# Performance work log

Hardware: AMD Instinct MI355X
Metric: run time of the kernel (lower is better)

## Reference

```python
import jax, jax.numpy as jnp
import numpy as np
from jax import lax

B, N_BASES, C_IN, C_OUT, K, HW = 32, 5, 128, 128, 3, 56

def setup_inputs() -> dict:
    key = jax.random.key(0)
    k1, k2, k3 = jax.random.split(key, 3)
    x = jax.random.normal(k1, (B, C_IN, HW, HW), dtype=jnp.float32)
    weights = jax.random.normal(k2, (N_BASES, C_OUT, C_IN, K, K), dtype=jnp.float32) * 0.05
    scales = jax.random.uniform(k3, (N_BASES,), dtype=jnp.float32)
    return {"x": x, "weights": weights, "scales": scales}

def _binarize(w):
    # per-base: sign(w) * mean(|w|) over the whole weight tensor of that base
    m = jnp.mean(jnp.abs(w), axis=(1, 2, 3, 4), keepdims=True)  # [N,1,1,1,1]
    return jnp.sign(w) * m

def reference(x, weights, scales):
    # torch pads with constant value 1 (not zero) once, then all bases share it
    xp = jnp.pad(x, ((0, 0), (0, 0), (1, 1), (1, 1)), constant_values=1.0)
    wq = _binarize(weights)                              # [N,O,I,K,K]
    wf = wq.reshape(N_BASES * C_OUT, C_IN, K, K)          # fuse bases into one conv
    out = lax.conv_general_dilated(
        xp, wf, window_strides=(1, 1), padding='VALID',
        dimension_numbers=('NCHW', 'OIHW', 'NCHW'))      # [B, N*O, H, W]
    out = out.reshape(B, N_BASES, C_OUT, HW, HW)
    return jnp.einsum('bnohw,n->bohw', out, scales)
```

## Files before the change

### kernel.cpp

```cpp
#include <hip/hip_runtime.h>
#include <stdint.h>

#define N_BASES 5
#define WELEM (128 * 128 * 3 * 3)

typedef __attribute__((ext_vector_type(4))) float f32x4;
typedef __attribute__((ext_vector_type(8))) short bf16x8;

__device__ __forceinline__ unsigned short f2bf(float v) {
  union { float f; uint32_t u; } un;
  un.f = v;
  uint32_t r = un.u + 0x7FFFu + ((un.u >> 16) & 1u);
  return (unsigned short)(r >> 16);
}

__device__ __forceinline__ void glds16(const void* g, void* l) {
  __builtin_amdgcn_global_load_lds(
      (const __attribute__((address_space(1))) void*)g,
      (__attribute__((address_space(3))) void*)l, 16, 0, 0);
}

__global__ __launch_bounds__(256) void prep_fused(
    const float* __restrict__ x, const float* __restrict__ w,
    unsigned short* __restrict__ xp, float* __restrict__ csum_part) {
  int bi = blockIdx.x;
  if (bi >= 1856) {
    int id = bi - 1856;
    int n = id >> 6;
    int chunk = id & 63;
    const f32x4* wb = (const f32x4*)(w + (size_t)n * WELEM + chunk * 2304);
    float s = 0.f;
    for (int i = threadIdx.x; i < 576; i += 256) {
      f32x4 v = wb[i];
      s += fabsf(v.x) + fabsf(v.y) + fabsf(v.z) + fabsf(v.w);
    }
    #pragma unroll
    for (int off = 32; off > 0; off >>= 1) s += __shfl_down(s, off);
    __shared__ float red[4];
    if ((threadIdx.x & 63) == 0) red[threadIdx.x >> 6] = s;
    __syncthreads();
    if (threadIdx.x == 0) csum_part[id] = red[0] + red[1] + red[2] + red[3];
    return;
  }
  int b = bi / 58;
  int hp = bi - b * 58;
  unsigned short* dst = xp + ((size_t)b * 58 + hp) * 58 * 128;
  int gh = hp - 1;
  if ((unsigned)gh >= 56u) {
    uint4 ones = make_uint4(0x3F803F80u, 0x3F803F80u, 0x3F803F80u, 0x3F803F80u);
    for (int i = threadIdx.x; i < 928; i += 256) ((uint4*)dst)[i] = ones;
    return;
  }
  __shared__ unsigned short tile[128][61];
  const float* src = x + ((size_t)b * 128 * 56 + gh) * 56;
  for (int i = threadIdx.x; i < 128 * 14; i += 256) {
    int c = i / 14;
    int k = i - c * 14;
    f32x4 v = *(const f32x4*)(src + (size_t)c * 3136 + k * 4);
    tile[c][1 + 4 * k + 0] = f2bf(v.x);
    tile[c][1 + 4 * k + 1] = f2bf(v.y);
    tile[c][1 + 4 * k + 2] = f2bf(v.z);
    tile[c][1 + 4 * k + 3] = f2bf(v.w);
  }
  if (threadIdx.x < 128) {
    tile[threadIdx.x][0] = 0x3F80;
    tile[threadIdx.x][57] = 0x3F80;
  }
  __syncthreads();
  for (int i = threadIdx.x; i < 928; i += 256) {
    int wp = i >> 4;
    int c8 = i & 15;
    union { uint4 q; unsigned short h[8]; } u;
    #pragma unroll
    for (int j = 0; j < 8; ++j) u.h[j] = tile[c8 * 8 + j][wp];
    *(uint4*)(dst + (size_t)wp * 128 + c8 * 8) = u.q;
  }
}

__global__ __launch_bounds__(256) void binweight_kernel(
    const float* __restrict__ w, const float* __restrict__ csum_part,
    const float* __restrict__ scales, unsigned short* __restrict__ wq) {
  __shared__ float parts[320];
  __shared__ float coef[N_BASES];
  for (int i = threadIdx.x; i < 320; i += 256) parts[i] = csum_part[i];
  __syncthreads();
  if (threadIdx.x < N_BASES) {
    float s = 0.f;
    #pragma unroll 8
    for (int k = 0; k < 64; ++k) s += parts[threadIdx.x * 64 + k];
    coef[threadIdx.x] = scales[threadIdx.x] * s * (1.0f / (float)WELEM);
  }
  __syncthreads();
  int f = blockIdx.x * 256 + threadIdx.x;
  float s = 0.f;
  #pragma unroll
  for (int n = 0; n < N_BASES; ++n) {
    float cn = coef[n];
    float v = w[n * WELEM + f];
    s += (v > 0.f) ? cn : ((v < 0.f) ? -cn : 0.f);
  }
  int o = f / 1152;
  int rem = f - o * 1152;
  int i = rem / 9;
  int t = rem - i * 9;
  int half = i >> 6;
  int c8 = (i >> 3) & 7;
  int e = i & 7;
  wq[(size_t)(t * 2 + half) * 8192 + o * 64 + ((c8 ^ (o & 7)) << 3) + e] = f2bf(s);
}

__global__ __launch_bounds__(256, 2) void conv_kernel(
    const unsigned short* __restrict__ xp, const unsigned short* __restrict__ wq,
    float* __restrict__ out) {
  __shared__ unsigned short patch[27648];
  __shared__ unsigned short btile[8192];

  const int tid = threadIdx.x;
  const int blk = blockIdx.x;
  const int pair = blk & 15;
  const int tileIdx = blk >> 4;
  const int hi = tileIdx >> 2;
  const int wi = tileIdx & 3;
  const int h0 = hi * 4;
  const int w0 = (wi == 3) ? 40 : wi * 16;

  const size_t rowstride = 58 * 128;
  for (int i = tid; i < 3456; i += 256) {
    int img = i / 1728;
    int r = i - img * 1728;
    int sp = r >> 4;
    int c16 = r & 15;
    int ph = sp / 18;
    int pw = sp - ph * 18;
    int b = pair + img * 16;
    const unsigned short* gp = xp + ((size_t)b * 58 + (h0 + ph)) * rowstride +
                               (size_t)(w0 + pw) * 128 + c16 * 8;
    uint4 v = *(const uint4*)gp;
    *(uint4*)&patch[img * 13824 + sp * 128 + ((c16 ^ (sp & 7)) << 3)] = v;
  }

  const int lane = tid & 63;
  const int wave = tid >> 6;
  const int img = wave >> 1;
  const int nh = wave & 1;
  const int l15 = lane & 15;
  const int quad = lane >> 4;

  f32x4 acc[4][4];
  #pragma unroll
  for (int mf = 0; mf < 4; ++mf)
    #pragma unroll
    for (int nf = 0; nf < 4; ++nf) acc[mf][nf] = (f32x4)0.f;

  const unsigned short* pb = &patch[img * 13824];

  #pragma unroll
  for (int t = 0; t < 9; ++t) {
    const int kh = t / 3;
    const int kw = t - kh * 3;
    int sp_mf[4];
    #pragma unroll
    for (int mf = 0; mf < 4; ++mf) sp_mf[mf] = (mf + kh) * 18 + (l15 + kw);
    #pragma unroll
    for (int half = 0; half < 2; ++half) {
      __syncthreads();
      {
        const unsigned short* g =
            wq + (size_t)(t * 2 + half) * 8192 + wave * 2048 + lane * 8;
        unsigned short* l = &btile[wave * 2048];
        #pragma unroll
        for (int j = 0; j < 4; ++j) glds16(g + j * 512, l + j * 512);
      }
      __syncthreads();
      #pragma unroll
      for (int kk = 0; kk < 2; ++kk) {
        const int kb = half * 2 + kk;
        bf16x8 af[4], bf[4];
        #pragma unroll
        for (int mf = 0; mf < 4; ++mf) {
          int sp = sp_mf[mf];
          af[mf] = *(const bf16x8*)&pb[sp * 128 + (((kb * 4 + quad) ^ (sp & 7)) << 3)];
        }
        #pragma unroll
        for (int nf = 0; nf < 4; ++nf) {
          int o = nh * 64 + nf * 16 + l15;
          bf[nf] = *(const bf16x8*)&btile[o * 64 + (((kk * 4 + quad) ^ (o & 7)) << 3)];
        }
        #pragma unroll
        for (int mf = 0; mf < 4; ++mf)
          #pragma unroll
          for (int nf = 0; nf < 4; ++nf)
            acc[mf][nf] = __builtin_amdgcn_mfma_f32_16x16x32_bf16(
                af[mf], bf[nf], acc[mf][nf], 0, 0, 0);
      }
    }
  }

  const int b = pair + img * 16;
  #pragma unroll
  for (int mf = 0; mf < 4; ++mf) {
    int h = h0 + mf;
    #pragma unroll
    for (int nf = 0; nf < 4; ++nf) {
      int o = nh * 64 + nf * 16 + l15;
      float* p = out + (((size_t)b * 128 + o) * 56 + h) * 56 + w0 + quad * 4;
      *(f32x4*)p = acc[mf][nf];
    }
  }
}

extern "C" void kernel_launch(void* const* d_in, const int* in_sizes, int n_in,
                              void* d_out, int out_size, void* d_ws, size_t ws_size,
                              hipStream_t stream) {
  const float* x = (const float*)d_in[0];
  const float* w = (const float*)d_in[1];
  const float* scales = (const float*)d_in[2];
  float* out = (float*)d_out;

  float* csum_part = (float*)d_ws;
  unsigned short* wq = (unsigned short*)((char*)d_ws + 4096);
  unsigned short* xpad = (unsigned short*)((char*)d_ws + 512 * 1024);

  prep_fused<<<1856 + 320, 256, 0, stream>>>(x, w, xpad, csum_part);
  binweight_kernel<<<576, 256, 0, stream>>>(w, csum_part, scales, wq);
  conv_kernel<<<56 * 16, 256, 0, stream>>>(xpad, wq, out);
}
```

Measured before the change: 152.4 us.

## Double-buffer conv weight tiles and retile blocks to one image by eight rows

Each conv block now covers one image and an 8-row output tile instead of two images at 4 rows each. This shrinks the input patch, since the halo rows are now shared across more output rows. Weight slices are double-buffered in LDS: the next slice is fetched with global_load_lds while the current one is consumed by MFMAs, and a single waitcnt plus barrier per step replaces the two __syncthreads. LDS use per block rises somewhat, and correctness now depends on the manual vmcnt wait and barrier placement.

Result: faster. 148.3 us (-2.7%).

```diff
diff --git a/kernel.cpp b/kernel.cpp
--- a/kernel.cpp
+++ b/kernel.cpp
@@ -112,36 +112,42 @@
 __global__ __launch_bounds__(256, 2) void conv_kernel(
     const unsigned short* __restrict__ xp, const unsigned short* __restrict__ wq,
     float* __restrict__ out) {
-  __shared__ unsigned short patch[27648];
-  __shared__ unsigned short btile[8192];
+  __shared__ unsigned short patch[23040];
+  __shared__ unsigned short btile[2][8192];
 
   const int tid = threadIdx.x;
   const int blk = blockIdx.x;
-  const int pair = blk & 15;
-  const int tileIdx = blk >> 4;
-  const int hi = tileIdx >> 2;
-  const int wi = tileIdx & 3;
-  const int h0 = hi * 4;
+  const int b = blk & 31;
+  const int tile = blk >> 5;
+  const int hi = tile >> 2;
+  const int wi = tile & 3;
+  const int h0 = hi * 8;
   const int w0 = (wi == 3) ? 40 : wi * 16;
 
+  const int lane = tid & 63;
+  const int wave = tid >> 6;
+
+  {
+    const unsigned short* g = wq + wave * 2048 + lane * 8;
+    unsigned short* l = &btile[0][wave * 2048];
+    #pragma unroll
+    for (int j = 0; j < 4; ++j) glds16(g + j * 512, l + j * 512);
+  }
+
   const size_t rowstride = 58 * 128;
-  for (int i = tid; i < 3456; i += 256) {
-    int img = i / 1728;
-    int r = i - img * 1728;
-    int sp = r >> 4;
-    int c16 = r & 15;
+  for (int i = tid; i < 2880; i += 256) {
+    int sp = i >> 4;
+    int c16 = i & 15;
     int ph = sp / 18;
     int pw = sp - ph * 18;
-    int b = pair + img * 16;
     const unsigned short* gp = xp + ((size_t)b * 58 + (h0 + ph)) * rowstride +
                                (size_t)(w0 + pw) * 128 + c16 * 8;
     uint4 v = *(const uint4*)gp;
-    *(uint4*)&patch[img * 13824 + sp * 128 + ((c16 ^ (sp & 7)) << 3)] = v;
-  }
-
-  const int lane = tid & 63;
-  const int wave = tid >> 6;
-  const int img = wave >> 1;
+    *(uint4*)&patch[sp * 128 + ((c16 ^ (sp & 7)) << 3)] = v;
+  }
+  __syncthreads();
+
+  const int mh = wave >> 1;
   const int nh = wave & 1;
   const int l15 = lane & 15;
   const int quad = lane >> 4;
@@ -151,8 +157,6 @@
   for (int mf = 0; mf < 4; ++mf)
     #pragma unroll
     for (int nf = 0; nf < 4; ++nf) acc[mf][nf] = (f32x4)0.f;
-
-  const unsigned short* pb = &patch[img * 13824];
 
   #pragma unroll
   for (int t = 0; t < 9; ++t) {
@@ -160,46 +164,52 @@
     const int kw = t - kh * 3;
     int sp_mf[4];
     #pragma unroll
-    for (int mf = 0; mf < 4; ++mf) sp_mf[mf] = (mf + kh) * 18 + (l15 + kw);
+    for (int mf = 0; mf < 4; ++mf)
+      sp_mf[mf] = (mh * 4 + mf + kh) * 18 + (l15 + kw);
     #pragma unroll
     for (int half = 0; half < 2; ++half) {
-      __syncthreads();
-      {
+      const int s = t * 2 + half;
+      if (s < 17) {
         const unsigned short* g =
-            wq + (size_t)(t * 2 + half) * 8192 + wave * 2048 + lane * 8;
-        unsigned short* l = &btile[wave * 2048];
+            wq + (size_t)(s + 1) * 8192 + wave * 2048 + lane * 8;
+        unsigned short* l = &btile[(s + 1) & 1][wave * 2048];
         #pragma unroll
         for (int j = 0; j < 4; ++j) glds16(g + j * 512, l + j * 512);
       }
-      __syncthreads();
+      const unsigned short* bt = btile[s & 1];
       #pragma unroll
       for (int kk = 0; kk < 2; ++kk) {
         const int kb = half * 2 + kk;
-        bf16x8 af[4], bf[4];
+        bf16x8 af[4], bfr[4];
         #pragma unroll
         for (int mf = 0; mf < 4; ++mf) {
           int sp = sp_mf[mf];
-          af[mf] = *(const bf16x8*)&pb[sp * 128 + (((kb * 4 + quad) ^ (sp & 7)) << 3)];
+          af[mf] = *(const bf16x8*)&patch[sp * 128 +
+                                          (((kb * 4 + quad) ^ (sp & 7)) << 3)];
         }
         #pragma unroll
         for (int nf = 0; nf < 4; ++nf) {
           int o = nh * 64 + nf * 16 + l15;
-          bf[nf] = *(const bf16x8*)&btile[o * 64 + (((kk * 4 + quad) ^ (o & 7)) << 3)];
+          bfr[nf] = *(const bf16x8*)&bt[o * 64 +
+                                        (((kk * 4 + quad) ^ (o & 7)) << 3)];
         }
         #pragma unroll
         for (int mf = 0; mf < 4; ++mf)
           #pragma unroll
           for (int nf = 0; nf < 4; ++nf)
             acc[mf][nf] = __builtin_amdgcn_mfma_f32_16x16x32_bf16(
-                af[mf], bf[nf], acc[mf][nf], 0, 0, 0);
+                af[mf], bfr[nf], acc[mf][nf], 0, 0, 0);
+      }
+      if (s < 17) {
+        asm volatile("s_waitcnt vmcnt(0)" ::: "memory");
+        asm volatile("s_barrier" ::: "memory");
       }
     }
   }
 
-  const int b = pair + img * 16;
   #pragma unroll
   for (int mf = 0; mf < 4; ++mf) {
-    int h = h0 + mf;
+    int h = h0 + mh * 4 + mf;
     #pragma unroll
     for (int nf = 0; nf < 4; ++nf) {
       int o = nh * 64 + nf * 16 + l15;
```
